# Kernel tuning notes

Measured on AMD Instinct MI355X. Metric: run time of the kernel, lower is better.

The kernel has to match this reference:

```python
import jax, jax.numpy as jnp
import numpy as np

MUL = 16            # multiplicity of 0e and 1o in irreps_in/irreps_out
N_NODES = 12500
N_EDGES = 200000
EDGE_ATTR_DIM = 16
WEIGHT_NUMEL = 4 * MUL * MUL  # 4 uvw paths, mul_sh = 1


def setup_inputs() -> dict:
    key = jax.random.key(0)
    ks = jax.random.split(key, 8)
    node_attr = jax.random.normal(ks[0], (N_NODES, 4 * MUL), dtype=jnp.float32)
    edge_index = jax.random.randint(ks[1], (2, N_EDGES), 0, N_NODES, dtype=jnp.int64)
    edge_attr = jax.random.normal(ks[2], (N_EDGES, EDGE_ATTR_DIM), dtype=jnp.float32)
    edge_sh = jax.random.normal(ks[3], (N_EDGES, 4), dtype=jnp.float32)
    # radial ScalarMLP params: Linear(16,16) + SiLU + Linear(16, weight_numel)
    s1 = 1.0 / np.sqrt(EDGE_ATTR_DIM)
    w1 = jax.random.uniform(ks[4], (EDGE_ATTR_DIM, EDGE_ATTR_DIM), jnp.float32, -s1, s1)
    b1 = jax.random.uniform(ks[5], (EDGE_ATTR_DIM,), jnp.float32, -s1, s1)
    w2 = jax.random.uniform(ks[6], (EDGE_ATTR_DIM, WEIGHT_NUMEL), jnp.float32, -s1, s1)
    b2 = jax.random.uniform(ks[7], (WEIGHT_NUMEL,), jnp.float32, -s1, s1)
    return {"node_attr": node_attr, "edge_index": edge_index, "edge_attr": edge_attr,
            "edge_sh": edge_sh, "w1": w1, "b1": b1, "w2": w2, "b2": b2}


def _conv(node_attr, edge_index, edge_attr, edge_sh, w1, b1, w2, b2):
    N = node_attr.shape[0]
    E = edge_attr.shape[0]
    src, dst = edge_index[0], edge_index[1]

    # gather source node features per edge
    x = node_attr[src]                         # [E, 4*MUL]
    x0 = x[:, :MUL]                            # [E, MUL]    (16x0e)
    x1 = x[:, MUL:].reshape(E, MUL, 3)         # [E, MUL, 3] (16x1o)
    y0 = edge_sh[:, 0]                         # [E]   (1x0e)
    y1 = edge_sh[:, 1:4]                       # [E,3] (1x1o)

    # radial MLP -> per-edge tensor-product weights
    h = jax.nn.silu(edge_attr @ w1 + b1)
    W = (h @ w2 + b2).reshape(E, 4, MUL, MUL)  # 4 uvw paths, [E,4,u,w]

    alpha = 1.0 / np.sqrt(2 * MUL).astype(np.float32)  # path norm: 2 paths * MUL fan-in per out irrep
    inv_sqrt3 = np.float32(1.0 / np.sqrt(3.0))

    # path 0: 0e x 0e -> 0e (CG = 1)
    out0 = jnp.einsum('eu,euw->ew', x0 * y0[:, None], W[:, 0])
    # path 1: 1o x 1o -> 0e (CG = delta_ij / sqrt(3), component-normalized)
    out0 = out0 + inv_sqrt3 * jnp.einsum('eui,ei,euw->ew', x1, y1, W[:, 1])
    # path 2: 0e x 1o -> 1o (CG = identity)
    out1 = jnp.einsum('eu,ei,euw->ewi', x0, y1, W[:, 2])
    # path 3: 1o x 0e -> 1o (CG = identity)
    out1 = out1 + jnp.einsum('eui,e,euw->ewi', x1, y0, W[:, 3])

    out_ij = jnp.concatenate([alpha * out0, (alpha * out1).reshape(E, 3 * MUL)], axis=-1)

    # scatter-mean into destination nodes
    sums = jax.ops.segment_sum(out_ij, dst, num_segments=N)
    counts = jax.ops.segment_sum(jnp.ones((E,), out_ij.dtype), dst, num_segments=N)
    return sums / jnp.maximum(counts, 1.0)[:, None]


def reference(node_attr, edge_index, edge_attr, edge_sh, w1, b1, w2, b2):
    return _conv(node_attr, edge_index, edge_attr, edge_sh, w1, b1, w2, b2)
```

## Files before the change

### kernel.cpp

```cpp
#include <hip/hip_runtime.h>
#include <math.h>

#define E_TOTAL  200000
#define NNODES   12500
#define OUT_ELEM 800000
#define NTILE    (E_TOTAL / 64)
#define PAD      64

typedef float    f32x4 __attribute__((ext_vector_type(4)));
typedef _Float16 f16x8 __attribute__((ext_vector_type(8)));
typedef _Float16 f16x4 __attribute__((ext_vector_type(4)));
typedef _Float16 f16x2 __attribute__((ext_vector_type(2)));

union AF { f16x8 f; f16x2 h2[4]; };

static const size_t OFF_CNT    = (size_t)NNODES * PAD * 64 * 2;
static const size_t OFF_BFRAG  = (OFF_CNT + (size_t)NNODES * 4 + 15) & ~(size_t)15;
static const size_t WS_NEEDED  = OFF_BFRAG + (size_t)36 * 64 * 8 * 2;

__global__ void k_prep(const float* __restrict__ w2, const float* __restrict__ b2,
                       int* __restrict__ cnt, _Float16* __restrict__ bfrag) {
    const int g = blockIdx.x * 256 + threadIdx.x;
    if (g < NNODES) cnt[g] = 0;
    if (g < 36 * 64) {
        const int slot = g >> 6, lane = g & 63;
        const int br = slot / 9, kb = slot - br * 9;
        const int quad = lane >> 4, n = lane & 15;
        const float alpha = 0.17677669529663687f;
        _Float16* dst = bfrag + (size_t)g * 8;
        #pragma unroll
        for (int j = 0; j < 8; ++j) {
            float v;
            if (kb < 8) {
                const int ku = kb * 32 + quad * 8 + j;
                v = w2[(ku >> 4) * 1024 + br * 256 + (ku & 15) * 16 + n];
            } else {
                const int loc = quad * 8 + j;
                v = (loc < 16) ? b2[br * 256 + loc * 16 + n] : 0.0f;
            }
            dst[j] = (_Float16)(alpha * v);
        }
    }
}

__global__ __launch_bounds__(256) void k_conv(
        const float* __restrict__ node_attr,
        const int*   __restrict__ edge_index,
        const float* __restrict__ edge_attr,
        const float* __restrict__ edge_sh,
        const float* __restrict__ w1,
        const float* __restrict__ b1,
        const f16x8* __restrict__ bfrag,
        int* __restrict__ cnt,
        _Float16* __restrict__ edge_out)
{
    const int t = threadIdx.x;
    __shared__ float  sh_h[64][17];
    __shared__ float4 sh_y[64];
    __shared__ _Float16 sh_s[6][64][24];
    __shared__ int sh_row[64];

    const int ebase = blockIdx.x * 64;
    const float inv_sqrt3 = 0.57735026918962576f;

    if (t < 64) {
        const int e2 = ebase + t;
        const int d = edge_index[E_TOTAL + e2];
        int slot = atomicAdd(&cnt[d], 1);
        if (slot >= PAD) slot = PAD - 1;
        sh_row[t] = d * PAD + slot;
    }

    {
        const int e_loc = t & 63, kq = t >> 6;
        const int e = ebase + e_loc;
        const float* ea = edge_attr + (size_t)e * 16;
        float ear[16];
        #pragma unroll
        for (int dq = 0; dq < 4; ++dq) {
            float4 v = *(const float4*)(ea + dq * 4);
            ear[dq * 4 + 0] = v.x; ear[dq * 4 + 1] = v.y;
            ear[dq * 4 + 2] = v.z; ear[dq * 4 + 3] = v.w;
        }
        float4 acc = *(const float4*)(b1 + kq * 4);
        #pragma unroll
        for (int d = 0; d < 16; ++d) {
            float4 wr = *(const float4*)(w1 + d * 16 + kq * 4);
            acc.x += ear[d] * wr.x; acc.y += ear[d] * wr.y;
            acc.z += ear[d] * wr.z; acc.w += ear[d] * wr.w;
        }
        sh_h[e_loc][kq * 4 + 0] = acc.x / (1.0f + __expf(-acc.x));
        sh_h[e_loc][kq * 4 + 1] = acc.y / (1.0f + __expf(-acc.y));
        sh_h[e_loc][kq * 4 + 2] = acc.z / (1.0f + __expf(-acc.z));
        sh_h[e_loc][kq * 4 + 3] = acc.w / (1.0f + __expf(-acc.w));
    }

    {
        const int e_loc = (t & 15) + ((t >> 6) << 4);
        const int pp = (t >> 4) & 3;
        const int u0 = pp * 4;
        const int e = ebase + e_loc;
        const int src = edge_index[e];
        const float4 yv = *(const float4*)(edge_sh + (size_t)e * 4);
        const float* xp = node_attr + (size_t)src * 64;
        float4 x0v = *(const float4*)(xp + u0);
        float x1v[4][3];
        #pragma unroll
        for (int q = 0; q < 4; ++q)
            #pragma unroll
            for (int i = 0; i < 3; ++i)
                x1v[q][i] = xp[16 + (u0 + q) * 3 + i];
        const float* x0p = &x0v.x;
        f16x4 s0h, s1h, x0h, ah, bh, ch;
        #pragma unroll
        for (int q = 0; q < 4; ++q) {
            s0h[q] = (_Float16)(x0p[q] * yv.x);
            s1h[q] = (_Float16)(inv_sqrt3 * (x1v[q][0] * yv.y + x1v[q][1] * yv.z + x1v[q][2] * yv.w));
            x0h[q] = (_Float16)x0p[q];
            ah[q]  = (_Float16)x1v[q][0];
            bh[q]  = (_Float16)x1v[q][1];
            ch[q]  = (_Float16)x1v[q][2];
        }
        *(f16x4*)&sh_s[0][e_loc][u0] = s0h;
        *(f16x4*)&sh_s[1][e_loc][u0] = s1h;
        *(f16x4*)&sh_s[2][e_loc][u0] = x0h;
        *(f16x4*)&sh_s[3][e_loc][u0] = ah;
        *(f16x4*)&sh_s[4][e_loc][u0] = bh;
        *(f16x4*)&sh_s[5][e_loc][u0] = ch;
        if (pp == 0) sh_y[e_loc] = yv;
    }
    __syncthreads();

    const int lane = t & 63, wv = t >> 6;
    const int m = lane & 15, quad = lane >> 4;
    const int e_loc = wv * 16 + m;
    const int qh = quad >> 1, ql = quad & 1;

    AF svh[6];
    #pragma unroll
    for (int b = 0; b < 6; ++b)
        svh[b].f = *(const f16x8*)&sh_s[b][e_loc][ql * 8];
    float hreg[8];
    #pragma unroll
    for (int kb = 0; kb < 8; ++kb) hreg[kb] = sh_h[e_loc][2 * kb + qh];

    f32x4 acc0  = {0.f, 0.f, 0.f, 0.f};
    f32x4 acc2  = {0.f, 0.f, 0.f, 0.f};
    f32x4 acc3a = {0.f, 0.f, 0.f, 0.f};
    f32x4 acc3b = {0.f, 0.f, 0.f, 0.f};
    f32x4 acc3c = {0.f, 0.f, 0.f, 0.f};

    for (int kb = 0; kb < 9; ++kb) {
        const f16x8 B0 = bfrag[(0 * 9 + kb) * 64 + lane];
        const f16x8 B1 = bfrag[(1 * 9 + kb) * 64 + lane];
        const f16x8 B2 = bfrag[(2 * 9 + kb) * 64 + lane];
        const f16x8 B3 = bfrag[(3 * 9 + kb) * 64 + lane];
        const float selF = (kb < 8) ? hreg[kb] : ((quad < 2) ? 1.0f : 0.0f);
        const _Float16 sh1 = (_Float16)selF;
        const f16x2 sel2 = (f16x2){sh1, sh1};
        AF A[6];
        #pragma unroll
        for (int b = 0; b < 6; ++b)
            #pragma unroll
            for (int p = 0; p < 4; ++p)
                A[b].h2[p] = sel2 * svh[b].h2[p];
        acc0  = __builtin_amdgcn_mfma_f32_16x16x32_f16(A[0].f, B0, acc0, 0, 0, 0);
        acc0  = __builtin_amdgcn_mfma_f32_16x16x32_f16(A[1].f, B1, acc0, 0, 0, 0);
        acc2  = __builtin_amdgcn_mfma_f32_16x16x32_f16(A[2].f, B2, acc2, 0, 0, 0);
        acc3a = __builtin_amdgcn_mfma_f32_16x16x32_f16(A[3].f, B3, acc3a, 0, 0, 0);
        acc3b = __builtin_amdgcn_mfma_f32_16x16x32_f16(A[4].f, B3, acc3b, 0, 0, 0);
        acc3c = __builtin_amdgcn_mfma_f32_16x16x32_f16(A[5].f, B3, acc3c, 0, 0, 0);
    }

    #pragma unroll
    for (int r = 0; r < 4; ++r) {
        const int el = wv * 16 + quad * 4 + r;
        const float4 yv = sh_y[el];
        const float t2v = acc2[r];
        const float o0 = acc0[r];
        const float oa = yv.y * t2v + yv.x * acc3a[r];
        const float ob = yv.z * t2v + yv.x * acc3b[r];
        const float oc = yv.w * t2v + yv.x * acc3c[r];
        f16x4 pk = {(_Float16)o0, (_Float16)oa, (_Float16)ob, (_Float16)oc};
        const size_t row = (size_t)sh_row[el];
        *(f16x4*)(edge_out + row * 64 + m * 4) = pk;
    }
}

__global__ __launch_bounds__(256) void k_gather(const _Float16* __restrict__ edge_out,
                                                const int* __restrict__ cnt,
                                                float* __restrict__ out) {
    __shared__ float sh_sum[4][64];
    const int t = threadIdx.x;
    const int lane = t & 63;
    const int wv = t >> 6;
    const int n = blockIdx.x * 4 + wv;
    int pe;
    if (lane < 16) pe = lane * 4;
    else { const int idx = lane - 16; const int w = idx / 3; pe = w * 4 + 1 + (idx - w * 3); }
    int c = cnt[n];
    if (c > PAD) c = PAD;
    const int ng = (c + 7) >> 3;
    const f16x8* base = (const f16x8*)(edge_out + (size_t)n * PAD * 64);
    const int rsub = lane >> 3;
    float acc[8] = {0.f, 0.f, 0.f, 0.f, 0.f, 0.f, 0.f, 0.f};
    for (int g = 0; g < ng; ++g) {
        const f16x8 v = base[g * 64 + lane];
        const int r = g * 8 + rsub;
        #pragma unroll
        for (int i = 0; i < 8; ++i)
            acc[i] += (r < c) ? (float)v[i] : 0.0f;
    }
    #pragma unroll
    for (int i = 0; i < 8; ++i) {
        acc[i] += __shfl_xor(acc[i], 8);
        acc[i] += __shfl_xor(acc[i], 16);
        acc[i] += __shfl_xor(acc[i], 32);
    }
    if (lane < 8) {
        #pragma unroll
        for (int i = 0; i < 8; ++i) sh_sum[wv][lane * 8 + i] = acc[i];
    }
    __syncthreads();
    const float s = sh_sum[wv][pe];
    out[n * 64 + lane] = s / (c > 0 ? (float)c : 1.0f);
}

__global__ void k_zero_f(float* __restrict__ out, float* __restrict__ counts) {
    int i = blockIdx.x * 256 + threadIdx.x;
    if (i < OUT_ELEM) out[i] = 0.0f;
    if (i < NNODES)   counts[i] = 0.0f;
}

#define EPB 80
#define NE  8
__global__ __launch_bounds__(256) void k_conv_atomic(
        const float* __restrict__ node_attr,
        const int*   __restrict__ edge_index,
        const float* __restrict__ edge_attr,
        const float* __restrict__ edge_sh,
        const float* __restrict__ w1,
        const float* __restrict__ b1,
        const float* __restrict__ w2,
        const float* __restrict__ b2,
        float* __restrict__ out,
        float* __restrict__ counts)
{
    const int thr   = threadIdx.x;
    const int lane  = thr & 63;
    const int wv    = thr >> 6;
    const int u     = lane >> 2;
    const int wbase = (lane & 3) * 4;

    float4 w2r[16];
    #pragma unroll
    for (int k = 0; k < 16; ++k)
        w2r[k] = *(const float4*)(w2 + k * 1024 + thr * 4);
    const float4 b2r = *(const float4*)(b2 + thr * 4);

    __shared__ __align__(16) float sh_h[NE][16];
    __shared__ float sh_s0[NE][16];
    __shared__ float sh_s1[NE][16];
    __shared__ float sh_x0[NE][16];
    __shared__ float sh_x1[NE][16][3];
    __shared__ float sh_y0[NE];
    __shared__ float sh_y1[NE][3];
    __shared__ int   sh_dst[NE];

    const float alpha     = 0.17677669529663687f;
    const float inv_sqrt3 = 0.57735026918962576f;
    const int e0 = blockIdx.x * EPB;

    for (int batch = 0; batch < EPB / NE; ++batch) {
        const int ebase = e0 + batch * NE;
        if (thr < 128) {
            const int le = thr >> 4, k = thr & 15;
            const int e = ebase + le;
            float acc = b1[k];
            const float* ea = edge_attr + (size_t)e * 16;
            #pragma unroll
            for (int d = 0; d < 16; ++d) acc += ea[d] * w1[d * 16 + k];
            sh_h[le][k] = acc / (1.0f + __expf(-acc));
            if (k == 0) sh_dst[le] = edge_index[E_TOTAL + e];
        } else {
            const int le = (thr - 128) >> 4, uu = thr & 15;
            const int e = ebase + le;
            const int src = edge_index[e];
            const float y0  = edge_sh[e * 4 + 0];
            const float y1a = edge_sh[e * 4 + 1];
            const float y1b = edge_sh[e * 4 + 2];
            const float y1c = edge_sh[e * 4 + 3];
            const float* xp = node_attr + (size_t)src * 64;
            const float x0v = xp[uu];
            const float xa = xp[16 + uu * 3 + 0];
            const float xb = xp[16 + uu * 3 + 1];
            const float xc = xp[16 + uu * 3 + 2];
            sh_x0[le][uu] = x0v;
            sh_x1[le][uu][0] = xa; sh_x1[le][uu][1] = xb; sh_x1[le][uu][2] = xc;
            sh_s0[le][uu] = x0v * y0;
            sh_s1[le][uu] = inv_sqrt3 * (xa * y1a + xb * y1b + xc * y1c);
            if (uu == 0) {
                sh_y0[le] = y0;
                sh_y1[le][0] = y1a; sh_y1[le][1] = y1b; sh_y1[le][2] = y1c;
            }
        }
        __syncthreads();

        for (int le = 0; le < NE; ++le) {
            float W0 = b2r.x, W1 = b2r.y, W2c = b2r.z, W3c = b2r.w;
            const float4* hv = (const float4*)sh_h[le];
            #pragma unroll
            for (int kk = 0; kk < 4; ++kk) {
                const float4 h4 = hv[kk];
                const int kb = kk * 4;
                W0  += h4.x * w2r[kb + 0].x; W1  += h4.x * w2r[kb + 0].y;
                W2c += h4.x * w2r[kb + 0].z; W3c += h4.x * w2r[kb + 0].w;
                W0  += h4.y * w2r[kb + 1].x; W1  += h4.y * w2r[kb + 1].y;
                W2c += h4.y * w2r[kb + 1].z; W3c += h4.y * w2r[kb + 1].w;
                W0  += h4.z * w2r[kb + 2].x; W1  += h4.z * w2r[kb + 2].y;
                W2c += h4.z * w2r[kb + 2].z; W3c += h4.z * w2r[kb + 2].w;
                W0  += h4.w * w2r[kb + 3].x; W1  += h4.w * w2r[kb + 3].y;
                W2c += h4.w * w2r[kb + 3].z; W3c += h4.w * w2r[kb + 3].w;
            }
            const int dst = sh_dst[le];
            float* op = out + (size_t)dst * 64;
            if (wv == 0 || wv == 1) {
                const float s = (wv == 0) ? sh_s0[le][u] : sh_s1[le][u];
                float v0 = s * W0, v1 = s * W1, v2 = s * W2c, v3 = s * W3c;
                #pragma unroll
                for (int off = 4; off <= 32; off <<= 1) {
                    v0 += __shfl_xor(v0, off); v1 += __shfl_xor(v1, off);
                    v2 += __shfl_xor(v2, off); v3 += __shfl_xor(v3, off);
                }
                if (lane < 4) {
                    atomicAdd(op + wbase + 0, alpha * v0);
                    atomicAdd(op + wbase + 1, alpha * v1);
                    atomicAdd(op + wbase + 2, alpha * v2);
                    atomicAdd(op + wbase + 3, alpha * v3);
                    if (wv == 0 && lane == 0) atomicAdd(&counts[dst], 1.0f);
                }
            } else if (wv == 2) {
                const float s = sh_x0[le][u];
                float v0 = s * W0, v1 = s * W1, v2 = s * W2c, v3 = s * W3c;
                #pragma unroll
                for (int off = 4; off <= 32; off <<= 1) {
                    v0 += __shfl_xor(v0, off); v1 += __shfl_xor(v1, off);
                    v2 += __shfl_xor(v2, off); v3 += __shfl_xor(v3, off);
                }
                if (lane < 4) {
                    const float ya = alpha * sh_y1[le][0];
                    const float yb = alpha * sh_y1[le][1];
                    const float yc = alpha * sh_y1[le][2];
                    float vv[4] = {v0, v1, v2, v3};
                    #pragma unroll
                    for (int q = 0; q < 4; ++q) {
                        float* qp = op + 16 + (wbase + q) * 3;
                        atomicAdd(qp + 0, vv[q] * ya);
                        atomicAdd(qp + 1, vv[q] * yb);
                        atomicAdd(qp + 2, vv[q] * yc);
                    }
                }
            } else {
                const float ay0 = alpha * sh_y0[le];
                #pragma unroll
                for (int i = 0; i < 3; ++i) {
                    const float s = sh_x1[le][u][i];
                    float v0 = s * W0, v1 = s * W1, v2 = s * W2c, v3 = s * W3c;
                    #pragma unroll
                    for (int off = 4; off <= 32; off <<= 1) {
                        v0 += __shfl_xor(v0, off); v1 += __shfl_xor(v1, off);
                        v2 += __shfl_xor(v2, off); v3 += __shfl_xor(v3, off);
                    }
                    if (lane < 4) {
                        atomicAdd(op + 16 + (wbase + 0) * 3 + i, ay0 * v0);
                        atomicAdd(op + 16 + (wbase + 1) * 3 + i, ay0 * v1);
                        atomicAdd(op + 16 + (wbase + 2) * 3 + i, ay0 * v2);
                        atomicAdd(op + 16 + (wbase + 3) * 3 + i, ay0 * v3);
                    }
                }
            }
        }
        __syncthreads();
    }
}

__global__ void k_div(float* __restrict__ out, const float* __restrict__ counts) {
    int i = blockIdx.x * 256 + threadIdx.x;
    if (i < OUT_ELEM) {
        float c = counts[i >> 6];
        out[i] *= 1.0f / fmaxf(c, 1.0f);
    }
}

extern "C" void kernel_launch(void* const* d_in, const int* in_sizes, int n_in,
                              void* d_out, int out_size, void* d_ws, size_t ws_size,
                              hipStream_t stream) {
    const float* node_attr  = (const float*)d_in[0];
    const int*   edge_index = (const int*)d_in[1];
    const float* edge_attr  = (const float*)d_in[2];
    const float* edge_sh    = (const float*)d_in[3];
    const float* w1         = (const float*)d_in[4];
    const float* b1         = (const float*)d_in[5];
    const float* w2         = (const float*)d_in[6];
    const float* b2         = (const float*)d_in[7];
    float* out = (float*)d_out;

    if (ws_size >= WS_NEEDED) {
        char* ws = (char*)d_ws;
        _Float16* edge_out = (_Float16*)ws;
        int*      cnt      = (int*)(ws + OFF_CNT);
        _Float16* bfrag    = (_Float16*)(ws + OFF_BFRAG);

        k_prep<<<(NNODES + 255) / 256, 256, 0, stream>>>(w2, b2, cnt, bfrag);
        k_conv<<<NTILE, 256, 0, stream>>>(
            node_attr, edge_index, edge_attr, edge_sh, w1, b1,
            (const f16x8*)bfrag, cnt, edge_out);
        k_gather<<<NNODES / 4, 256, 0, stream>>>(edge_out, cnt, out);
    } else {
        float* counts = (float*)d_ws;
        k_zero_f<<<(OUT_ELEM + 255) / 256, 256, 0, stream>>>(out, counts);
        k_conv_atomic<<<E_TOTAL / EPB, 256, 0, stream>>>(
            node_attr, edge_index, edge_attr, edge_sh, w1, b1, w2, b2, out, counts);
        k_div<<<(OUT_ELEM + 255) / 256, 256, 0, stream>>>(out, counts);
    }
}
```

Before: 134.9 us.

## Make k_conv wave-local: drop block barrier, shuffle row/sh values, vectorize gathers

```diff
diff --git a/kernel.cpp b/kernel.cpp
--- a/kernel.cpp
+++ b/kernel.cpp
@@ -43,7 +43,7 @@
     }
 }
 
-__global__ __launch_bounds__(256) void k_conv(
+__global__ __launch_bounds__(256, 4) void k_conv(
         const float* __restrict__ node_attr,
         const int*   __restrict__ edge_index,
         const float* __restrict__ edge_attr,
@@ -55,25 +55,36 @@
         _Float16* __restrict__ edge_out)
 {
     const int t = threadIdx.x;
-    __shared__ float  sh_h[64][17];
-    __shared__ float4 sh_y[64];
-    __shared__ _Float16 sh_s[6][64][24];
-    __shared__ int sh_row[64];
-
-    const int ebase = blockIdx.x * 64;
+    const int wv = t >> 6, lane = t & 63;
+    const int m = lane & 15, hi = lane >> 4;
+
+    __shared__ float    sh_h[4][16][17];
+    __shared__ _Float16 sh_s[4][6][16][24];
+
+    const int ebw = blockIdx.x * 64 + wv * 16;
     const float inv_sqrt3 = 0.57735026918962576f;
 
-    if (t < 64) {
-        const int e2 = ebase + t;
+    int myrow = 0;
+    if (lane < 16) {
+        const int e2 = ebw + lane;
         const int d = edge_index[E_TOTAL + e2];
         int slot = atomicAdd(&cnt[d], 1);
         if (slot >= PAD) slot = PAD - 1;
-        sh_row[t] = d * PAD + slot;
-    }
+        myrow = d * PAD + slot;
+    }
+
+    const int e = ebw + m;
+
+    const int src = edge_index[e];
+    const float4 yv = *(const float4*)(edge_sh + (size_t)e * 4);
+    const int u0 = hi * 4;
+    const float* xp = node_attr + (size_t)src * 64;
+    const float4 x0v = *(const float4*)(xp + u0);
+    float4 x1q[3];
+    #pragma unroll
+    for (int q = 0; q < 3; ++q) x1q[q] = *(const float4*)(xp + 16 + u0 * 3 + q * 4);
 
     {
-        const int e_loc = t & 63, kq = t >> 6;
-        const int e = ebase + e_loc;
         const float* ea = edge_attr + (size_t)e * 16;
         float ear[16];
         #pragma unroll
@@ -82,67 +93,52 @@
             ear[dq * 4 + 0] = v.x; ear[dq * 4 + 1] = v.y;
             ear[dq * 4 + 2] = v.z; ear[dq * 4 + 3] = v.w;
         }
-        float4 acc = *(const float4*)(b1 + kq * 4);
+        float4 acc = *(const float4*)(b1 + hi * 4);
         #pragma unroll
         for (int d = 0; d < 16; ++d) {
-            float4 wr = *(const float4*)(w1 + d * 16 + kq * 4);
+            float4 wr = *(const float4*)(w1 + d * 16 + hi * 4);
             acc.x += ear[d] * wr.x; acc.y += ear[d] * wr.y;
             acc.z += ear[d] * wr.z; acc.w += ear[d] * wr.w;
         }
-        sh_h[e_loc][kq * 4 + 0] = acc.x / (1.0f + __expf(-acc.x));
-        sh_h[e_loc][kq * 4 + 1] = acc.y / (1.0f + __expf(-acc.y));
-        sh_h[e_loc][kq * 4 + 2] = acc.z / (1.0f + __expf(-acc.z));
-        sh_h[e_loc][kq * 4 + 3] = acc.w / (1.0f + __expf(-acc.w));
+        sh_h[wv][m][hi * 4 + 0] = acc.x / (1.0f + __expf(-acc.x));
+        sh_h[wv][m][hi * 4 + 1] = acc.y / (1.0f + __expf(-acc.y));
+        sh_h[wv][m][hi * 4 + 2] = acc.z / (1.0f + __expf(-acc.z));
+        sh_h[wv][m][hi * 4 + 3] = acc.w / (1.0f + __expf(-acc.w));
     }
 
     {
-        const int e_loc = (t & 15) + ((t >> 6) << 4);
-        const int pp = (t >> 4) & 3;
-        const int u0 = pp * 4;
-        const int e = ebase + e_loc;
-        const int src = edge_index[e];
-        const float4 yv = *(const float4*)(edge_sh + (size_t)e * 4);
-        const float* xp = node_attr + (size_t)src * 64;
-        float4 x0v = *(const float4*)(xp + u0);
-        float x1v[4][3];
-        #pragma unroll
-        for (int q = 0; q < 4; ++q)
-            #pragma unroll
-            for (int i = 0; i < 3; ++i)
-                x1v[q][i] = xp[16 + (u0 + q) * 3 + i];
-        const float* x0p = &x0v.x;
+        const float x0p[4] = {x0v.x, x0v.y, x0v.z, x0v.w};
+        const float x1p[12] = {x1q[0].x, x1q[0].y, x1q[0].z, x1q[0].w,
+                               x1q[1].x, x1q[1].y, x1q[1].z, x1q[1].w,
+                               x1q[2].x, x1q[2].y, x1q[2].z, x1q[2].w};
         f16x4 s0h, s1h, x0h, ah, bh, ch;
         #pragma unroll
         for (int q = 0; q < 4; ++q) {
+            const float xa = x1p[q * 3 + 0], xb = x1p[q * 3 + 1], xc = x1p[q * 3 + 2];
             s0h[q] = (_Float16)(x0p[q] * yv.x);
-            s1h[q] = (_Float16)(inv_sqrt3 * (x1v[q][0] * yv.y + x1v[q][1] * yv.z + x1v[q][2] * yv.w));
+            s1h[q] = (_Float16)(inv_sqrt3 * (xa * yv.y + xb * yv.z + xc * yv.w));
             x0h[q] = (_Float16)x0p[q];
-            ah[q]  = (_Float16)x1v[q][0];
-            bh[q]  = (_Float16)x1v[q][1];
-            ch[q]  = (_Float16)x1v[q][2];
-        }
-        *(f16x4*)&sh_s[0][e_loc][u0] = s0h;
-        *(f16x4*)&sh_s[1][e_loc][u0] = s1h;
-        *(f16x4*)&sh_s[2][e_loc][u0] = x0h;
-        *(f16x4*)&sh_s[3][e_loc][u0] = ah;
-        *(f16x4*)&sh_s[4][e_loc][u0] = bh;
-        *(f16x4*)&sh_s[5][e_loc][u0] = ch;
-        if (pp == 0) sh_y[e_loc] = yv;
-    }
-    __syncthreads();
-
-    const int lane = t & 63, wv = t >> 6;
-    const int m = lane & 15, quad = lane >> 4;
-    const int e_loc = wv * 16 + m;
-    const int qh = quad >> 1, ql = quad & 1;
+            ah[q]  = (_Float16)xa;
+            bh[q]  = (_Float16)xb;
+            ch[q]  = (_Float16)xc;
+        }
+        *(f16x4*)&sh_s[wv][0][m][u0] = s0h;
+        *(f16x4*)&sh_s[wv][1][m][u0] = s1h;
+        *(f16x4*)&sh_s[wv][2][m][u0] = x0h;
+        *(f16x4*)&sh_s[wv][3][m][u0] = ah;
+        *(f16x4*)&sh_s[wv][4][m][u0] = bh;
+        *(f16x4*)&sh_s[wv][5][m][u0] = ch;
+    }
+
+    const int qh = hi >> 1, ql = hi & 1;
 
     AF svh[6];
     #pragma unroll
     for (int b = 0; b < 6; ++b)
-        svh[b].f = *(const f16x8*)&sh_s[b][e_loc][ql * 8];
+        svh[b].f = *(const f16x8*)&sh_s[wv][b][m][ql * 8];
     float hreg[8];
     #pragma unroll
-    for (int kb = 0; kb < 8; ++kb) hreg[kb] = sh_h[e_loc][2 * kb + qh];
+    for (int kb = 0; kb < 8; ++kb) hreg[kb] = sh_h[wv][m][2 * kb + qh];
 
     f32x4 acc0  = {0.f, 0.f, 0.f, 0.f};
     f32x4 acc2  = {0.f, 0.f, 0.f, 0.f};
@@ -150,12 +146,13 @@
     f32x4 acc3b = {0.f, 0.f, 0.f, 0.f};
     f32x4 acc3c = {0.f, 0.f, 0.f, 0.f};
 
+    #pragma unroll
     for (int kb = 0; kb < 9; ++kb) {
         const f16x8 B0 = bfrag[(0 * 9 + kb) * 64 + lane];
         const f16x8 B1 = bfrag[(1 * 9 + kb) * 64 + lane];
         const f16x8 B2 = bfrag[(2 * 9 + kb) * 64 + lane];
         const f16x8 B3 = bfrag[(3 * 9 + kb) * 64 + lane];
-        const float selF = (kb < 8) ? hreg[kb] : ((quad < 2) ? 1.0f : 0.0f);
+        const float selF = (kb < 8) ? hreg[kb] : ((hi < 2) ? 1.0f : 0.0f);
         const _Float16 sh1 = (_Float16)selF;
         const f16x2 sel2 = (f16x2){sh1, sh1};
         AF A[6];
@@ -174,16 +171,19 @@
 
     #pragma unroll
     for (int r = 0; r < 4; ++r) {
-        const int el = wv * 16 + quad * 4 + r;
-        const float4 yv = sh_y[el];
+        const int el = hi * 4 + r;
+        const int   row = __shfl(myrow, el);
+        const float y0s = __shfl(yv.x, el);
+        const float y1s = __shfl(yv.y, el);
+        const float y2s = __shfl(yv.z, el);
+        const float y3s = __shfl(yv.w, el);
         const float t2v = acc2[r];
         const float o0 = acc0[r];
-        const float oa = yv.y * t2v + yv.x * acc3a[r];
-        const float ob = yv.z * t2v + yv.x * acc3b[r];
-        const float oc = yv.w * t2v + yv.x * acc3c[r];
+        const float oa = y1s * t2v + y0s * acc3a[r];
+        const float ob = y2s * t2v + y0s * acc3b[r];
+        const float oc = y3s * t2v + y0s * acc3c[r];
         f16x4 pk = {(_Float16)o0, (_Float16)oa, (_Float16)ob, (_Float16)oc};
-        const size_t row = (size_t)sh_row[el];
-        *(f16x4*)(edge_out + row * 64 + m * 4) = pk;
+        *(f16x4*)(edge_out + (size_t)row * 64 + m * 4) = pk;
     }
 }
 
```

Result: slower. 138.5 us (+2.6%).
